# Performance work log

Hardware: AMD Instinct MI355X
Metric: run time of the kernel (lower is better)

Reference implementation:

```python
import jax, jax.numpy as jnp
import numpy as np

EMBED_DIM = 1024
NUM_HEADS = 16
HEAD_DIM = EMBED_DIM // NUM_HEADS
SCALE = 1.0 / np.sqrt(HEAD_DIM).astype(np.float32)


def setup_inputs() -> dict:
    key = jax.random.key(0)
    ks = jax.random.split(key, 9)
    B, T, C = 2, 2048, EMBED_DIM
    s = 1.0 / np.sqrt(C).astype(np.float32)  # torch Linear init scale (approx, uniform bound)
    return {
        "x_q": jax.random.normal(ks[0], (B, T, C), dtype=jnp.float32),
        "attn_mask": jnp.zeros((T, T), dtype=jnp.float32),
        "Wq": jax.random.uniform(ks[1], (C, C), jnp.float32, -s, s),
        "bq": jax.random.uniform(ks[2], (C,), jnp.float32, -s, s),
        "Wk": jax.random.uniform(ks[3], (C, C), jnp.float32, -s, s),
        "bk": jax.random.uniform(ks[4], (C,), jnp.float32, -s, s),
        "Wv": jax.random.uniform(ks[5], (C, C), jnp.float32, -s, s),
        "bv": jax.random.uniform(ks[6], (C,), jnp.float32, -s, s),
        "Wo": jax.random.uniform(ks[7], (C, C), jnp.float32, -s, s),
        "bo": jax.random.uniform(ks[8], (C,), jnp.float32, -s, s),
    }


def reference(x_q, attn_mask, Wq, bq, Wk, bk, Wv, bv, Wo, bo):
    B, Tq, C = x_q.shape
    # self-attention: x_kv = x_q
    q = (x_q @ Wq.T + bq).reshape(B, Tq, NUM_HEADS, HEAD_DIM)
    k = (x_q @ Wk.T + bk).reshape(B, Tq, NUM_HEADS, HEAD_DIM)
    v = (x_q @ Wv.T + bv).reshape(B, Tq, NUM_HEADS, HEAD_DIM)
    # (B, H, Tq, Tk)
    scores = jnp.einsum('bqhd,bkhd->bhqk', q, k) * SCALE
    scores = scores + attn_mask[None, None, :, :]  # 2D additive mask path
    attn = jax.nn.softmax(scores, axis=-1)  # dropout p=0.0 -> identity
    out = jnp.einsum('bhqk,bkhd->bqhd', attn, v).reshape(B, Tq, C)
    out = out @ Wo.T + bo
    return out
```

## Files before the change

kernel.cpp:

```cpp
#include <hip/hip_runtime.h>
#include <hip/hip_bf16.h>
#include <stdint.h>

typedef _Float16 f16x8_t __attribute__((ext_vector_type(8)));
typedef _Float16 f16x4_t __attribute__((ext_vector_type(4)));
typedef float    f32x4_t __attribute__((ext_vector_type(4)));

#define T_SEQ 2048
#define NH    16
#define HD    64
#define CDIM  1024
#define NTOK  4096
#define SCALE_F 0.125f

__device__ __forceinline__ void async_ld16(void* lds, const void* g) {
    __builtin_amdgcn_global_load_lds(
        (const __attribute__((address_space(1))) uint32_t*)g,
        (__attribute__((address_space(3))) uint32_t*)lds, 16, 0, 0);
}

__global__ __launch_bounds__(256) void cvt_f32_f16(const float* __restrict__ src,
                                                   _Float16* __restrict__ dst, int n4) {
    int i = blockIdx.x * blockDim.x + threadIdx.x;
    if (i < n4) {
        float4 v = ((const float4*)src)[i];
        f16x4_t h;
        h[0] = (_Float16)v.x; h[1] = (_Float16)v.y;
        h[2] = (_Float16)v.z; h[3] = (_Float16)v.w;
        ((f16x4_t*)dst)[i] = h;
    }
}

__global__ __launch_bounds__(256) void mask_flag_k(const float* __restrict__ mask, int n4,
                                                   int* __restrict__ flag) {
    int i = blockIdx.x * blockDim.x + threadIdx.x;
    int stride = gridDim.x * blockDim.x;
    int any = 0;
    for (; i < n4; i += stride) {
        float4 v = ((const float4*)mask)[i];
        any |= (v.x != 0.f) | (v.y != 0.f) | (v.z != 0.f) | (v.w != 0.f);
    }
    if (any) atomicOr(flag, 1);
}

template<int MODE>
__global__ __launch_bounds__(256)
void gemm_f16(const _Float16* __restrict__ Ag, const _Float16* __restrict__ Bg,
              const float* __restrict__ b0, const float* __restrict__ b1,
              const float* __restrict__ b2,
              _Float16* __restrict__ Qo, _Float16* __restrict__ Ko,
              _Float16* __restrict__ Vto, float* __restrict__ Fo)
{
    __shared__ _Float16 sA[128 * 32];
    __shared__ _Float16 sB[128 * 32];
    const int K = CDIM;
    const int tid  = threadIdx.x;
    const int lane = tid & 63, wv = tid >> 6;
    const int wr = wv >> 1, wc = wv & 1;
    const int rowA0 = blockIdx.x * 128;
    const int rowB0 = blockIdx.y * 128;
    const int srow = lane >> 2;
    const int scol = (lane & 3) * 8;
    const int fr = lane & 15, fg = lane >> 4;
    f32x4_t acc[4][4] = {};

    for (int k0 = 0; k0 < K; k0 += 32) {
#pragma unroll
        for (int i = 0; i < 2; ++i) {
            const int eoff = i * 2048 + wv * 512;
            const int r = (eoff >> 5) + srow;
            async_ld16(&sA[eoff], Ag + (size_t)(rowA0 + r) * K + k0 + scol);
            async_ld16(&sB[eoff], Bg + (size_t)(rowB0 + r) * K + k0 + scol);
        }
        __syncthreads();
        f16x8_t a[4], b[4];
#pragma unroll
        for (int mi = 0; mi < 4; ++mi)
            a[mi] = *(const f16x8_t*)&sA[(wr * 64 + mi * 16 + fr) * 32 + fg * 8];
#pragma unroll
        for (int ni = 0; ni < 4; ++ni)
            b[ni] = *(const f16x8_t*)&sB[(wc * 64 + ni * 16 + fr) * 32 + fg * 8];
#pragma unroll
        for (int mi = 0; mi < 4; ++mi)
#pragma unroll
            for (int ni = 0; ni < 4; ++ni)
                acc[mi][ni] = __builtin_amdgcn_mfma_f32_16x16x32_f16(a[mi], b[ni], acc[mi][ni], 0, 0, 0);
        __syncthreads();
    }

#pragma unroll
    for (int mi = 0; mi < 4; ++mi) {
#pragma unroll
        for (int ni = 0; ni < 4; ++ni) {
            const int col = rowB0 + wc * 64 + ni * 16 + fr;
#pragma unroll
            for (int r = 0; r < 4; ++r) {
                const int row = rowA0 + wr * 64 + mi * 16 + fg * 4 + r;
                float v = acc[mi][ni][r];
                if (MODE == 0) {
                    const int which = col >> 10, cc = col & 1023;
                    const float* bp = (which == 0) ? b0 : ((which == 1) ? b1 : b2);
                    v += bp[cc];
                    const int bb = row >> 11, t = row & (T_SEQ - 1);
                    const int h = cc >> 6, d = cc & 63;
                    const int bh = bb * NH + h;
                    if (which == 0)
                        Qo[((size_t)bh * T_SEQ + t) * HD + d] = (_Float16)(v * SCALE_F);
                    else if (which == 1)
                        Ko[((size_t)bh * T_SEQ + t) * HD + d] = (_Float16)v;
                    else
                        Vto[((size_t)bh * HD + d) * T_SEQ + t] = (_Float16)v;
                } else {
                    Fo[(size_t)row * CDIM + col] = v + b0[col];
                }
            }
        }
    }
}

__global__ __launch_bounds__(512)
void attn_f16(const _Float16* __restrict__ Q, const _Float16* __restrict__ Kg,
              const _Float16* __restrict__ Vt, const float* __restrict__ mask,
              const int* __restrict__ mflag, _Float16* __restrict__ AO)
{
    __shared__ __align__(16) _Float16 sK[2][4096];
    __shared__ __align__(16) _Float16 sV[2][4096];
    __shared__ __align__(16) _Float16 Ps[8][16][72];

    const int tid = threadIdx.x;
    const int lane = tid & 63, wv = tid >> 6;
    const int fr = lane & 15, fg = lane >> 4;
    const int bh = blockIdx.y;
    const int b = bh >> 4, h = bh & (NH - 1);
    const int q0 = blockIdx.x * 128 + wv * 16;
    const _Float16* Qb = Q  + (size_t)bh * T_SEQ * HD;
    const _Float16* Kb = Kg + (size_t)bh * T_SEQ * HD;
    const _Float16* Vb = Vt + (size_t)bh * HD * T_SEQ;

    const int srow = wv * 8 + ((lane >> 3) & 7);
    const int ssw  = ((lane & 7) * 8) ^ ((srow & 7) << 3);
    const int rsw  = (fr & 7) << 3;

    f16x8_t qf[2];
#pragma unroll
    for (int dc = 0; dc < 2; ++dc)
        qf[dc] = *(const f16x8_t*)&Qb[(size_t)(q0 + fr) * HD + dc * 32 + fg * 8];

    f32x4_t o[4] = {};
    float m_run = -1e30f, l_run = 0.f;
    const int mf = mflag[0];

    async_ld16(&sK[0][wv * 512], Kb + (size_t)srow * HD + ssw);
    async_ld16(&sV[0][wv * 512], Vb + (size_t)srow * T_SEQ + 0 + ssw);

    for (int t = 0; t < T_SEQ / 64; ++t) {
        const int k0 = t * 64, cur = t & 1;
        __syncthreads();
        if (t + 1 < T_SEQ / 64) {
            const int kn = k0 + 64, nb = cur ^ 1;
            async_ld16(&sK[nb][wv * 512], Kb + (size_t)(kn + srow) * HD + ssw);
            async_ld16(&sV[nb][wv * 512], Vb + (size_t)srow * T_SEQ + kn + ssw);
        }

        f32x4_t s[4];
#pragma unroll
        for (int kt = 0; kt < 4; ++kt) {
            const int krow = (kt * 16 + fr) * 64;
            f16x8_t kf0 = *(const f16x8_t*)&sK[cur][krow + ((fg * 8) ^ rsw)];
            f16x8_t kf1 = *(const f16x8_t*)&sK[cur][krow + ((32 + fg * 8) ^ rsw)];
            f32x4_t z = {};
            z = __builtin_amdgcn_mfma_f32_16x16x32_f16(kf0, qf[0], z, 0, 0, 0);
            s[kt] = __builtin_amdgcn_mfma_f32_16x16x32_f16(kf1, qf[1], z, 0, 0, 0);
        }
        if (mf) {
            const float* mrow = mask + (size_t)(q0 + fr) * T_SEQ + k0;
#pragma unroll
            for (int kt = 0; kt < 4; ++kt)
#pragma unroll
                for (int r = 0; r < 4; ++r)
                    s[kt][r] += mrow[kt * 16 + fg * 4 + r];
        }

        float tmax = -1e30f;
#pragma unroll
        for (int kt = 0; kt < 4; ++kt) {
            float a = fmaxf(fmaxf(s[kt][0], s[kt][1]), fmaxf(s[kt][2], s[kt][3]));
            tmax = fmaxf(tmax, a);
        }
        tmax = fmaxf(tmax, __shfl_xor(tmax, 16, 64));
        tmax = fmaxf(tmax, __shfl_xor(tmax, 32, 64));

        if (!__all(tmax <= m_run + 5.0f)) {
            const float mnew = fmaxf(m_run, tmax);
            const float sc = __expf(m_run - mnew);
            m_run = mnew;
            float scq[4];
#pragma unroll
            for (int r = 0; r < 4; ++r)
                scq[r] = __shfl(sc, fg * 4 + r, 64);
#pragma unroll
            for (int df = 0; df < 4; ++df)
#pragma unroll
                for (int r = 0; r < 4; ++r)
                    o[df][r] *= scq[r];
            l_run *= sc;
        }

        float rs = 0.f;
#pragma unroll
        for (int kt = 0; kt < 4; ++kt) {
#pragma unroll
            for (int r = 0; r < 4; ++r) {
                s[kt][r] = __expf(s[kt][r] - m_run);
                rs += s[kt][r];
            }
            f16x4_t hp;
            hp[0] = (_Float16)s[kt][0]; hp[1] = (_Float16)s[kt][1];
            hp[2] = (_Float16)s[kt][2]; hp[3] = (_Float16)s[kt][3];
            *(f16x4_t*)&Ps[wv][fr][kt * 16 + fg * 4] = hp;
        }
        rs += __shfl_xor(rs, 16, 64);
        rs += __shfl_xor(rs, 32, 64);
        l_run += rs;

        asm volatile("s_waitcnt lgkmcnt(0)" ::: "memory");
        __builtin_amdgcn_sched_barrier(0);

#pragma unroll
        for (int kt2 = 0; kt2 < 2; ++kt2) {
            f16x8_t pa = *(const f16x8_t*)&Ps[wv][fr][kt2 * 32 + fg * 8];
#pragma unroll
            for (int df = 0; df < 4; ++df) {
                f16x8_t vb = *(const f16x8_t*)&sV[cur][(df * 16 + fr) * 64 + ((kt2 * 32 + fg * 8) ^ rsw)];
                o[df] = __builtin_amdgcn_mfma_f32_16x16x32_f16(pa, vb, o[df], 0, 0, 0);
            }
        }
    }

    float lq[4];
#pragma unroll
    for (int r = 0; r < 4; ++r)
        lq[r] = __shfl(l_run, fg * 4 + r, 64);
#pragma unroll
    for (int r = 0; r < 4; ++r) {
        const float inv = 1.f / lq[r];
        const size_t row = (size_t)(b * T_SEQ + q0 + fg * 4 + r);
#pragma unroll
        for (int df = 0; df < 4; ++df)
            AO[row * CDIM + h * HD + df * 16 + fr] = (_Float16)(o[df][r] * inv);
    }
}

extern "C" void kernel_launch(void* const* d_in, const int* in_sizes, int n_in,
                              void* d_out, int out_size, void* d_ws, size_t ws_size,
                              hipStream_t stream) {
    const float* x    = (const float*)d_in[0];
    const float* mask = (const float*)d_in[1];
    const float* Wq   = (const float*)d_in[2];
    const float* bq   = (const float*)d_in[3];
    const float* Wk   = (const float*)d_in[4];
    const float* bk   = (const float*)d_in[5];
    const float* Wv   = (const float*)d_in[6];
    const float* bv   = (const float*)d_in[7];
    const float* Wo   = (const float*)d_in[8];
    const float* bo   = (const float*)d_in[9];
    float* out = (float*)d_out;

    char* ws = (char*)d_ws;
    _Float16* xh    = (_Float16*)(ws);
    _Float16* Wqkvh = (_Float16*)(ws + (8u  << 20));
    _Float16* Woh   = (_Float16*)(ws + (14u << 20));
    _Float16* Qp    = (_Float16*)(ws + (16u << 20));
    _Float16* Kp    = (_Float16*)(ws + (24u << 20));
    _Float16* Vtp   = (_Float16*)(ws + (32u << 20));
    int* mflag      = (int*)(ws + (40u << 20));
    _Float16* AO    = xh;

    hipMemsetAsync(mflag, 0, 4, stream);
    cvt_f32_f16<<<4096, 256, 0, stream>>>(x, xh, NTOK * CDIM / 4);
    cvt_f32_f16<<<1024, 256, 0, stream>>>(Wq, Wqkvh,                   CDIM * CDIM / 4);
    cvt_f32_f16<<<1024, 256, 0, stream>>>(Wk, Wqkvh + CDIM * CDIM,     CDIM * CDIM / 4);
    cvt_f32_f16<<<1024, 256, 0, stream>>>(Wv, Wqkvh + 2 * CDIM * CDIM, CDIM * CDIM / 4);
    cvt_f32_f16<<<1024, 256, 0, stream>>>(Wo, Woh, CDIM * CDIM / 4);
    mask_flag_k<<<512, 256, 0, stream>>>(mask, T_SEQ * T_SEQ / 4, mflag);

    gemm_f16<0><<<dim3(32, 24), 256, 0, stream>>>(xh, Wqkvh, bq, bk, bv,
                                                  Qp, Kp, Vtp, nullptr);
    attn_f16<<<dim3(16, 32), 512, 0, stream>>>(Qp, Kp, Vtp, mask, mflag, AO);
    gemm_f16<1><<<dim3(32, 8), 256, 0, stream>>>(AO, Woh, bo, nullptr, nullptr,
                                                 nullptr, nullptr, nullptr, out);
}
```

Baseline: 147.3 us.

## Fuse prep kernels, double-buffer GEMM, pre-tile K/V layout, use exp2 softmax

```diff
diff --git a/kernel.cpp b/kernel.cpp
--- a/kernel.cpp
+++ b/kernel.cpp
@@ -11,7 +11,8 @@
 #define HD    64
 #define CDIM  1024
 #define NTOK  4096
-#define SCALE_F 0.125f
+#define QSCALE 0.18033688011112042f
+#define LOG2E  1.4426950408889634f
 
 __device__ __forceinline__ void async_ld16(void* lds, const void* g) {
     __builtin_amdgcn_global_load_lds(
@@ -19,28 +20,32 @@
         (__attribute__((address_space(3))) uint32_t*)lds, 16, 0, 0);
 }
 
-__global__ __launch_bounds__(256) void cvt_f32_f16(const float* __restrict__ src,
-                                                   _Float16* __restrict__ dst, int n4) {
-    int i = blockIdx.x * blockDim.x + threadIdx.x;
-    if (i < n4) {
-        float4 v = ((const float4*)src)[i];
-        f16x4_t h;
-        h[0] = (_Float16)v.x; h[1] = (_Float16)v.y;
-        h[2] = (_Float16)v.z; h[3] = (_Float16)v.w;
-        ((f16x4_t*)dst)[i] = h;
-    }
-}
-
-__global__ __launch_bounds__(256) void mask_flag_k(const float* __restrict__ mask, int n4,
-                                                   int* __restrict__ flag) {
-    int i = blockIdx.x * blockDim.x + threadIdx.x;
-    int stride = gridDim.x * blockDim.x;
-    int any = 0;
-    for (; i < n4; i += stride) {
-        float4 v = ((const float4*)mask)[i];
-        any |= (v.x != 0.f) | (v.y != 0.f) | (v.z != 0.f) | (v.w != 0.f);
-    }
-    if (any) atomicOr(flag, 1);
+__global__ __launch_bounds__(256)
+void prep_all(const float* __restrict__ x, const float* __restrict__ Wq,
+              const float* __restrict__ Wk, const float* __restrict__ Wv,
+              const float* __restrict__ Wo, const float* __restrict__ mask,
+              _Float16* __restrict__ xh, _Float16* __restrict__ Wqkvh,
+              _Float16* __restrict__ Woh, int* __restrict__ flag)
+{
+    const int XQ = NTOK * CDIM / 4;
+    const int WQ = CDIM * CDIM / 4;
+    int i = blockIdx.x * 256 + threadIdx.x;
+    if (i < XQ + 4 * WQ) {
+        const float* s; _Float16* d; int off;
+        if (i < XQ) { s = x; d = xh; off = i; }
+        else {
+            int j = i - XQ; int w = j >> 18; off = j & (WQ - 1);
+            s = (w == 0) ? Wq : (w == 1) ? Wk : (w == 2) ? Wv : Wo;
+            d = (w == 3) ? Woh : Wqkvh + (size_t)w * CDIM * CDIM;
+        }
+        float4 v = ((const float4*)s)[off];
+        f16x4_t h = {(_Float16)v.x, (_Float16)v.y, (_Float16)v.z, (_Float16)v.w};
+        ((f16x4_t*)d)[off] = h;
+    } else {
+        int off = i - (XQ + 4 * WQ);
+        float4 v = ((const float4*)mask)[off];
+        if (v.x != 0.f || v.y != 0.f || v.z != 0.f || v.w != 0.f) atomicOr(flag, 1);
+    }
 }
 
 template<int MODE>
@@ -51,8 +56,8 @@
               _Float16* __restrict__ Qo, _Float16* __restrict__ Ko,
               _Float16* __restrict__ Vto, float* __restrict__ Fo)
 {
-    __shared__ _Float16 sA[128 * 32];
-    __shared__ _Float16 sB[128 * 32];
+    __shared__ _Float16 sA[2][128 * 32];
+    __shared__ _Float16 sB[2][128 * 32];
     const int K = CDIM;
     const int tid  = threadIdx.x;
     const int lane = tid & 63, wv = tid >> 6;
@@ -64,29 +69,34 @@
     const int fr = lane & 15, fg = lane >> 4;
     f32x4_t acc[4][4] = {};
 
+#define STAGE(buf, kk) do {                                                     \
+        _Pragma("unroll")                                                       \
+        for (int i_ = 0; i_ < 2; ++i_) {                                        \
+            const int eoff = i_ * 2048 + wv * 512;                              \
+            const int r_ = i_ * 64 + wv * 16 + srow;                            \
+            async_ld16(&sA[buf][eoff], Ag + (size_t)(rowA0 + r_) * K + (kk) + scol); \
+            async_ld16(&sB[buf][eoff], Bg + (size_t)(rowB0 + r_) * K + (kk) + scol); \
+        } } while (0)
+
+    STAGE(0, 0);
     for (int k0 = 0; k0 < K; k0 += 32) {
-#pragma unroll
-        for (int i = 0; i < 2; ++i) {
-            const int eoff = i * 2048 + wv * 512;
-            const int r = (eoff >> 5) + srow;
-            async_ld16(&sA[eoff], Ag + (size_t)(rowA0 + r) * K + k0 + scol);
-            async_ld16(&sB[eoff], Bg + (size_t)(rowB0 + r) * K + k0 + scol);
-        }
+        const int cur = (k0 >> 5) & 1;
         __syncthreads();
+        if (k0 + 32 < K) STAGE(cur ^ 1, k0 + 32);
         f16x8_t a[4], b[4];
 #pragma unroll
         for (int mi = 0; mi < 4; ++mi)
-            a[mi] = *(const f16x8_t*)&sA[(wr * 64 + mi * 16 + fr) * 32 + fg * 8];
+            a[mi] = *(const f16x8_t*)&sA[cur][(wr * 64 + mi * 16 + fr) * 32 + fg * 8];
 #pragma unroll
         for (int ni = 0; ni < 4; ++ni)
-            b[ni] = *(const f16x8_t*)&sB[(wc * 64 + ni * 16 + fr) * 32 + fg * 8];
+            b[ni] = *(const f16x8_t*)&sB[cur][(wc * 64 + ni * 16 + fr) * 32 + fg * 8];
 #pragma unroll
         for (int mi = 0; mi < 4; ++mi)
 #pragma unroll
             for (int ni = 0; ni < 4; ++ni)
                 acc[mi][ni] = __builtin_amdgcn_mfma_f32_16x16x32_f16(a[mi], b[ni], acc[mi][ni], 0, 0, 0);
-        __syncthreads();
-    }
+    }
+#undef STAGE
 
 #pragma unroll
     for (int mi = 0; mi < 4; ++mi) {
@@ -101,15 +111,16 @@
                     const int which = col >> 10, cc = col & 1023;
                     const float* bp = (which == 0) ? b0 : ((which == 1) ? b1 : b2);
                     v += bp[cc];
-                    const int bb = row >> 11, t = row & (T_SEQ - 1);
+                    const int bb = row >> 11, tt = row & (T_SEQ - 1);
                     const int h = cc >> 6, d = cc & 63;
                     const int bh = bb * NH + h;
+                    const size_t tbase = ((size_t)bh * 32 + (tt >> 6)) * 4096;
                     if (which == 0)
-                        Qo[((size_t)bh * T_SEQ + t) * HD + d] = (_Float16)(v * SCALE_F);
+                        Qo[((size_t)bh * T_SEQ + tt) * HD + d] = (_Float16)(v * QSCALE);
                     else if (which == 1)
-                        Ko[((size_t)bh * T_SEQ + t) * HD + d] = (_Float16)v;
+                        Ko[tbase + (size_t)(d >> 3) * 512 + (tt & 63) * 8 + (d & 7)] = (_Float16)v;
                     else
-                        Vto[((size_t)bh * HD + d) * T_SEQ + t] = (_Float16)v;
+                        Vto[tbase + (size_t)((tt >> 3) & 7) * 512 + d * 8 + (tt & 7)] = (_Float16)v;
                 } else {
                     Fo[(size_t)row * CDIM + col] = v + b0[col];
                 }
@@ -118,14 +129,14 @@
     }
 }
 
-__global__ __launch_bounds__(512)
-void attn_f16(const _Float16* __restrict__ Q, const _Float16* __restrict__ Kg,
-              const _Float16* __restrict__ Vt, const float* __restrict__ mask,
+__global__ __launch_bounds__(512, 4)
+void attn_f16(const _Float16* __restrict__ Q, const _Float16* __restrict__ Kc,
+              const _Float16* __restrict__ Vc, const float* __restrict__ mask,
               const int* __restrict__ mflag, _Float16* __restrict__ AO)
 {
     __shared__ __align__(16) _Float16 sK[2][4096];
     __shared__ __align__(16) _Float16 sV[2][4096];
-    __shared__ __align__(16) _Float16 Ps[8][16][72];
+    __shared__ __align__(16) _Float16 Ps[8][1024];
 
     const int tid = threadIdx.x;
     const int lane = tid & 63, wv = tid >> 6;
@@ -133,13 +144,10 @@
     const int bh = blockIdx.y;
     const int b = bh >> 4, h = bh & (NH - 1);
     const int q0 = blockIdx.x * 128 + wv * 16;
-    const _Float16* Qb = Q  + (size_t)bh * T_SEQ * HD;
-    const _Float16* Kb = Kg + (size_t)bh * T_SEQ * HD;
-    const _Float16* Vb = Vt + (size_t)bh * HD * T_SEQ;
-
-    const int srow = wv * 8 + ((lane >> 3) & 7);
-    const int ssw  = ((lane & 7) * 8) ^ ((srow & 7) << 3);
-    const int rsw  = (fr & 7) << 3;
+    const _Float16* Qb  = Q  + (size_t)bh * T_SEQ * HD;
+    const _Float16* Kbh = Kc + (size_t)bh * (T_SEQ * HD);
+    const _Float16* Vbh = Vc + (size_t)bh * (T_SEQ * HD);
+    const int soff = wv * 512 + lane * 8;
 
     f16x8_t qf[2];
 #pragma unroll
@@ -150,49 +158,55 @@
     float m_run = -1e30f, l_run = 0.f;
     const int mf = mflag[0];
 
-    async_ld16(&sK[0][wv * 512], Kb + (size_t)srow * HD + ssw);
-    async_ld16(&sV[0][wv * 512], Vb + (size_t)srow * T_SEQ + 0 + ssw);
+    async_ld16(&sK[0][wv * 512], Kbh + soff);
+    async_ld16(&sV[0][wv * 512], Vbh + soff);
 
     for (int t = 0; t < T_SEQ / 64; ++t) {
-        const int k0 = t * 64, cur = t & 1;
+        const int cur = t & 1;
         __syncthreads();
         if (t + 1 < T_SEQ / 64) {
-            const int kn = k0 + 64, nb = cur ^ 1;
-            async_ld16(&sK[nb][wv * 512], Kb + (size_t)(kn + srow) * HD + ssw);
-            async_ld16(&sV[nb][wv * 512], Vb + (size_t)srow * T_SEQ + kn + ssw);
+            async_ld16(&sK[cur ^ 1][wv * 512], Kbh + (t + 1) * 4096 + soff);
+            async_ld16(&sV[cur ^ 1][wv * 512], Vbh + (t + 1) * 4096 + soff);
         }
 
         f32x4_t s[4];
+        __builtin_amdgcn_s_setprio(1);
 #pragma unroll
         for (int kt = 0; kt < 4; ++kt) {
-            const int krow = (kt * 16 + fr) * 64;
-            f16x8_t kf0 = *(const f16x8_t*)&sK[cur][krow + ((fg * 8) ^ rsw)];
-            f16x8_t kf1 = *(const f16x8_t*)&sK[cur][krow + ((32 + fg * 8) ^ rsw)];
+            f16x8_t kf0 = *(const f16x8_t*)&sK[cur][fg * 512       + (kt * 16 + fr) * 8];
+            f16x8_t kf1 = *(const f16x8_t*)&sK[cur][(4 + fg) * 512 + (kt * 16 + fr) * 8];
             f32x4_t z = {};
-            z = __builtin_amdgcn_mfma_f32_16x16x32_f16(kf0, qf[0], z, 0, 0, 0);
+            z     = __builtin_amdgcn_mfma_f32_16x16x32_f16(kf0, qf[0], z, 0, 0, 0);
             s[kt] = __builtin_amdgcn_mfma_f32_16x16x32_f16(kf1, qf[1], z, 0, 0, 0);
         }
+        __builtin_amdgcn_s_setprio(0);
+
+        f16x8_t vb[2][4];
+#pragma unroll
+        for (int kt2 = 0; kt2 < 2; ++kt2)
+#pragma unroll
+            for (int df = 0; df < 4; ++df)
+                vb[kt2][df] = *(const f16x8_t*)&sV[cur][(kt2 * 4 + fg) * 512 + (df * 16 + fr) * 8];
+
         if (mf) {
-            const float* mrow = mask + (size_t)(q0 + fr) * T_SEQ + k0;
+            const float* mrow = mask + (size_t)(q0 + fr) * T_SEQ + t * 64;
 #pragma unroll
             for (int kt = 0; kt < 4; ++kt)
 #pragma unroll
                 for (int r = 0; r < 4; ++r)
-                    s[kt][r] += mrow[kt * 16 + fg * 4 + r];
+                    s[kt][r] += mrow[kt * 16 + fg * 4 + r] * LOG2E;
         }
 
         float tmax = -1e30f;
 #pragma unroll
-        for (int kt = 0; kt < 4; ++kt) {
-            float a = fmaxf(fmaxf(s[kt][0], s[kt][1]), fmaxf(s[kt][2], s[kt][3]));
-            tmax = fmaxf(tmax, a);
-        }
+        for (int kt = 0; kt < 4; ++kt)
+            tmax = fmaxf(tmax, fmaxf(fmaxf(s[kt][0], s[kt][1]), fmaxf(s[kt][2], s[kt][3])));
         tmax = fmaxf(tmax, __shfl_xor(tmax, 16, 64));
         tmax = fmaxf(tmax, __shfl_xor(tmax, 32, 64));
 
-        if (!__all(tmax <= m_run + 5.0f)) {
+        if (!__all(tmax <= m_run + 8.0f)) {
             const float mnew = fmaxf(m_run, tmax);
-            const float sc = __expf(m_run - mnew);
+            const float sc = __builtin_amdgcn_exp2f(m_run - mnew);
             m_run = mnew;
             float scq[4];
 #pragma unroll
@@ -209,15 +223,14 @@
         float rs = 0.f;
 #pragma unroll
         for (int kt = 0; kt < 4; ++kt) {
+            f16x4_t hp;
 #pragma unroll
             for (int r = 0; r < 4; ++r) {
-                s[kt][r] = __expf(s[kt][r] - m_run);
-                rs += s[kt][r];
+                const float p = __builtin_amdgcn_exp2f(s[kt][r] - m_run);
+                rs += p;
+                hp[r] = (_Float16)p;
             }
-            f16x4_t hp;
-            hp[0] = (_Float16)s[kt][0]; hp[1] = (_Float16)s[kt][1];
-            hp[2] = (_Float16)s[kt][2]; hp[3] = (_Float16)s[kt][3];
-            *(f16x4_t*)&Ps[wv][fr][kt * 16 + fg * 4] = hp;
+            *(f16x4_t*)&Ps[wv][(kt * 2 + (fg >> 1)) * 128 + fr * 8 + (fg & 1) * 4] = hp;
         }
         rs += __shfl_xor(rs, 16, 64);
         rs += __shfl_xor(rs, 32, 64);
@@ -226,15 +239,15 @@
         asm volatile("s_waitcnt lgkmcnt(0)" ::: "memory");
         __builtin_amdgcn_sched_barrier(0);
 
+        __builtin_amdgcn_s_setprio(1);
 #pragma unroll
         for (int kt2 = 0; kt2 < 2; ++kt2) {
-            f16x8_t pa = *(const f16x8_t*)&Ps[wv][fr][kt2 * 32 + fg * 8];
-#pragma unroll
-            for (int df = 0; df < 4; ++df) {
-                f16x8_t vb = *(const f16x8_t*)&sV[cur][(df * 16 + fr) * 64 + ((kt2 * 32 + fg * 8) ^ rsw)];
-                o[df] = __builtin_amdgcn_mfma_f32_16x16x32_f16(pa, vb, o[df], 0, 0, 0);
-            }
-        }
+            f16x8_t pa = *(const f16x8_t*)&Ps[wv][(kt2 * 4 + fg) * 128 + fr * 8];
+#pragma unroll
+            for (int df = 0; df < 4; ++df)
+                o[df] = __builtin_amdgcn_mfma_f32_16x16x32_f16(pa, vb[kt2][df], o[df], 0, 0, 0);
+        }
+        __builtin_amdgcn_s_setprio(0);
     }
 
     float lq[4];
@@ -271,22 +284,16 @@
     _Float16* Wqkvh = (_Float16*)(ws + (8u  << 20));
     _Float16* Woh   = (_Float16*)(ws + (14u << 20));
     _Float16* Qp    = (_Float16*)(ws + (16u << 20));
-    _Float16* Kp    = (_Float16*)(ws + (24u << 20));
-    _Float16* Vtp   = (_Float16*)(ws + (32u << 20));
+    _Float16* Kc    = (_Float16*)(ws + (24u << 20));
+    _Float16* Vc    = (_Float16*)(ws + (32u << 20));
     int* mflag      = (int*)(ws + (40u << 20));
     _Float16* AO    = xh;
 
     hipMemsetAsync(mflag, 0, 4, stream);
-    cvt_f32_f16<<<4096, 256, 0, stream>>>(x, xh, NTOK * CDIM / 4);
-    cvt_f32_f16<<<1024, 256, 0, stream>>>(Wq, Wqkvh,                   CDIM * CDIM / 4);
-    cvt_f32_f16<<<1024, 256, 0, stream>>>(Wk, Wqkvh + CDIM * CDIM,     CDIM * CDIM / 4);
-    cvt_f32_f16<<<1024, 256, 0, stream>>>(Wv, Wqkvh + 2 * CDIM * CDIM, CDIM * CDIM / 4);
-    cvt_f32_f16<<<1024, 256, 0, stream>>>(Wo, Woh, CDIM * CDIM / 4);
-    mask_flag_k<<<512, 256, 0, stream>>>(mask, T_SEQ * T_SEQ / 4, mflag);
-
+    prep_all<<<12288, 256, 0, stream>>>(x, Wq, Wk, Wv, Wo, mask, xh, Wqkvh, Woh, mflag);
     gemm_f16<0><<<dim3(32, 24), 256, 0, stream>>>(xh, Wqkvh, bq, bk, bv,
-                                                  Qp, Kp, Vtp, nullptr);
-    attn_f16<<<dim3(16, 32), 512, 0, stream>>>(Qp, Kp, Vtp, mask, mflag, AO);
+                                                  Qp, Kc, Vc, nullptr);
+    attn_f16<<<dim3(16, 32), 512, 0, stream>>>(Qp, Kc, Vc, mask, mflag, AO);
     gemm_f16<1><<<dim3(32, 8), 256, 0, stream>>>(AO, Woh, bo, nullptr, nullptr,
                                                  nullptr, nullptr, nullptr, out);
 }
```

Result: faster. 134.4 us (-8.7%).
